# Kernel optimization log

Measured on AMD Instinct MI355X. Metric: run time of the kernel, lower is better.

## Reference

```python
import jax, jax.numpy as jnp
import numpy as np

N_NODES = 100000
N_EDGES = 600000
IN_F, HID_F, OUT_F = 128, 128, 64


def setup_inputs() -> dict:
    key = jax.random.key(0)
    ks = jax.random.split(key, 12)
    s = 0.05  # small init scale to keep activations bounded
    return {
        "features": jax.random.normal(ks[0], (N_NODES, IN_F), jnp.float32),
        "edge_src": jax.random.randint(ks[1], (N_EDGES,), 0, N_NODES, jnp.int32),
        "edge_dst": jax.random.randint(ks[2], (N_EDGES,), 0, N_NODES, jnp.int32),
        "W1": jax.random.normal(ks[3], (HID_F, 3 * IN_F), jnp.float32) * s,
        "b1": jnp.zeros((HID_F,), jnp.float32),
        "bn_gamma": jnp.ones((HID_F,), jnp.float32),
        "bn_beta": jnp.zeros((HID_F,), jnp.float32),
        "bn_mean": jnp.zeros((HID_F,), jnp.float32),
        "bn_var": jnp.ones((HID_F,), jnp.float32),
        "W3": jax.random.normal(ks[4], (HID_F, 3 * HID_F), jnp.float32) * s,
        "b3": jnp.zeros((HID_F,), jnp.float32),
        "Wm1": jax.random.normal(ks[5], (HID_F, HID_F), jnp.float32) * s,
        "bm1": jnp.zeros((HID_F,), jnp.float32),
        "Wm2": jax.random.normal(ks[6], (OUT_F, HID_F), jnp.float32) * s,
        "bm2": jnp.zeros((OUT_F,), jnp.float32),
    }


def _cheb_conv(x, W, b, src, dst, dinv, n):
    """DGL ChebConv with k=3, lambda_max=2 (re_norm=1).
    L f = f - D^-1/2 A D^-1/2 f  via gather-scatter on the edge list."""
    def lap(f):
        agg = jax.ops.segment_sum((f * dinv)[src], dst, num_segments=n)
        return f - agg * dinv
    X0 = x
    X1 = -lap(X0)                 # X1 = -re_norm*L(X0) + (re_norm-1)*X0, re_norm=1
    X2 = -2.0 * lap(X1) - X0      # X2 = -2*re_norm*L(X1) + 2*(re_norm-1)*X1 - X0
    Xt = jnp.concatenate([X0, X1, X2], axis=1)  # [n, 3*in]
    return Xt @ W.T + b


def reference(features, edge_src, edge_dst, W1, b1, bn_gamma, bn_beta,
              bn_mean, bn_var, W3, b3, Wm1, bm1, Wm2, bm2):
    n = features.shape[0]
    deg = jax.ops.segment_sum(jnp.ones_like(edge_dst, jnp.float32), edge_dst,
                              num_segments=n)
    dinv = jnp.clip(deg, 1.0, None) ** -0.5  # D^{-1/2}, in-degree (DGL)
    dinv = dinv[:, None]

    x = jax.nn.relu(_cheb_conv(features, W1, b1, edge_src, edge_dst, dinv, n))
    # BatchNorm1d (eval mode)
    x = (x - bn_mean) * jax.lax.rsqrt(bn_var + 1e-5) * bn_gamma + bn_beta
    # NOTE: original early-stopping loop never updates x -> dead code, omitted.
    x_res = x
    x = jax.nn.relu(_cheb_conv(x, W3, b3, edge_src, edge_dst, dinv, n))
    x = x + x_res  # dropout is identity in eval mode
    # MLP head
    h = jax.nn.relu(x @ Wm1.T + bm1)
    return h @ Wm2.T + bm2
```

## Files before the change

### kernel.cpp

```cpp
#include <hip/hip_runtime.h>
#include <cstdint>
#include <cstddef>

#define NF 128
#define SCAN_B 256

typedef __attribute__((ext_vector_type(4))) float f32x4;
typedef __attribute__((ext_vector_type(8))) short bf16x8;

#define GL2LDS16(g, l) __builtin_amdgcn_global_load_lds(                     \
    (const __attribute__((address_space(1))) unsigned*)(g),                  \
    (__attribute__((address_space(3))) unsigned*)(l), 16, 0, 0)

static __device__ inline float bf2f(short u) {
    union { unsigned u; float f; } v;
    v.u = ((unsigned)(unsigned short)u) << 16;
    return v.f;
}
static __device__ inline short f2bf(float f) {
    union { float f; unsigned u; } v; v.f = f;
    unsigned r = v.u + 0x7FFF + ((v.u >> 16) & 1);
    return (short)(r >> 16);
}
static __device__ inline float u2f(unsigned u) {
    union { unsigned u; float f; } v; v.u = u; return v.f;
}
static __device__ inline unsigned f2u(float f) {
    union { float f; unsigned u; } v; v.f = f; return v.u;
}
static __device__ inline unsigned packbf(float lo, float hi) {
    unsigned ul = f2u(lo), uh = f2u(hi);
    ul = ul + 0x7FFF + ((ul >> 16) & 1);
    uh = uh + 0x7FFF + ((uh >> 16) & 1);
    return (ul >> 16) | (uh & 0xFFFF0000u);
}


static __global__ __launch_bounds__(256) void k_pro(
    const int* __restrict__ dst, int ne, int* __restrict__ counts,
    const float* __restrict__ feat, short* __restrict__ fbf, int n8, int nbE, int nbF,
    const float* __restrict__ w1, const float* __restrict__ w3,
    const float* __restrict__ wm1, const float* __restrict__ wm2,
    short* __restrict__ o1, short* __restrict__ o3,
    short* __restrict__ om1, short* __restrict__ om2) {
    int b = blockIdx.x;
    if (b < nbE) {
        int e = b * 256 + threadIdx.x;
        if (e < ne) atomicAdd(&counts[dst[e]], 1);
        return;
    }
    b -= nbE;
    if (b < nbF) {
        int i = b * 256 + threadIdx.x;
        if (i < n8) {
            f32x4 a = *(const f32x4*)&feat[(size_t)i * 8];
            f32x4 c = *(const f32x4*)&feat[(size_t)i * 8 + 4];
            bf16x8 r;
            r[0] = f2bf(a[0]); r[1] = f2bf(a[1]); r[2] = f2bf(a[2]); r[3] = f2bf(a[3]);
            r[4] = f2bf(c[0]); r[5] = f2bf(c[1]); r[6] = f2bf(c[2]); r[7] = f2bf(c[3]);
            *(bf16x8*)&fbf[(size_t)i * 8] = r;
        }
        return;
    }
    b -= nbF;
    int i = b * 256 + threadIdx.x;
    if (i < 12288) {
        const float* x = (i < 6144) ? w1 : w3;
        short* y       = (i < 6144) ? o1 : o3;
        int ii = (i < 6144) ? i : i - 6144;
        int r = ii / 48, c = ii % 48;
        int kt = c * 8, seg = kt >> 7, o = kt & 127;
        const float* base = x + (size_t)r * 384;
        float c0, c1, c2;
        if (seg == 0)      { c0 = 1.f;  c1 = -1.f; c2 = 1.f;  }
        else if (seg == 1) { c0 = 0.f;  c1 = 1.f;  c2 = -4.f; }
        else               { c0 = 0.f;  c1 = 0.f;  c2 = 2.f;  }
        bf16x8 rr;
#pragma unroll
        for (int h = 0; h < 2; ++h) {
            f32x4 a0 = *(const f32x4*)&base[o + h * 4];
            f32x4 a1 = *(const f32x4*)&base[128 + o + h * 4];
            f32x4 a2 = *(const f32x4*)&base[256 + o + h * 4];
#pragma unroll
            for (int j = 0; j < 4; ++j)
                rr[h * 4 + j] = f2bf(c0 * a0[j] + c1 * a1[j] + c2 * a2[j]);
        }
        *(bf16x8*)&y[(size_t)r * 384 + kt] = rr;
        return;
    }
    const float* x; short* y; int off;
    if (i < 14336) { x = wm1; y = om1; off = i - 12288; }
    else           { x = wm2; y = om2; off = i - 14336; }
    f32x4 a = *(const f32x4*)&x[(size_t)off * 8];
    f32x4 c = *(const f32x4*)&x[(size_t)off * 8 + 4];
    bf16x8 r;
    r[0] = f2bf(a[0]); r[1] = f2bf(a[1]); r[2] = f2bf(a[2]); r[3] = f2bf(a[3]);
    r[4] = f2bf(c[0]); r[5] = f2bf(c[1]); r[6] = f2bf(c[2]); r[7] = f2bf(c[3]);
    *(bf16x8*)&y[(size_t)off * 8] = r;
}


static __global__ void k_scan1(const int* __restrict__ counts, int n,
                               int* __restrict__ row_off, int* __restrict__ bsum) {
    __shared__ int s[SCAN_B];
    int t = threadIdx.x;
    int base = blockIdx.x * SCAN_B;
    int v = (base + t < n) ? counts[base + t] : 0;
    s[t] = v;
    __syncthreads();
    for (int off = 1; off < SCAN_B; off <<= 1) {
        int x = 0;
        if (t >= off) x = s[t - off];
        __syncthreads();
        if (t >= off) s[t] += x;
        __syncthreads();
    }
    if (base + t < n) row_off[base + t] = s[t] - v;
    if (t == SCAN_B - 1) bsum[blockIdx.x] = s[t];
}

static __global__ void k_scan2(int* __restrict__ bsum, int nb) {
    __shared__ int s[512];
    int t = threadIdx.x;
    int v = (t < nb) ? bsum[t] : 0;
    s[t] = v;
    __syncthreads();
    for (int off = 1; off < 512; off <<= 1) {
        int x = 0;
        if (t >= off) x = s[t - off];
        __syncthreads();
        if (t >= off) s[t] += x;
        __syncthreads();
    }
    if (t < nb) bsum[t] = s[t] - v;
}

static __global__ void k_scan3(int* __restrict__ row_off, const int* __restrict__ bsum,
                               int n, int ne, int* __restrict__ cursor,
                               const int* __restrict__ counts, float* __restrict__ dinv) {
    int i = blockIdx.x * SCAN_B + threadIdx.x;
    if (i < n) {
        int v = row_off[i] + bsum[blockIdx.x];
        row_off[i] = v;
        cursor[i] = v;
        float d = fmaxf((float)counts[i], 1.0f);
        dinv[i] = rsqrtf(d);
    }
    if (i == 0) row_off[n] = ne;
}

static __global__ void k_fill(const int* __restrict__ src, const int* __restrict__ dst, int ne,
                              int* __restrict__ cursor, int* __restrict__ csr) {
    int e = blockIdx.x * blockDim.x + threadIdx.x;
    if (e < ne) {
        int d = dst[e];
        int p = atomicAdd(&cursor[d], 1);
        csr[p] = src[e];
    }
}


static __global__ __launch_bounds__(256) void k_lap(
    const short* __restrict__ Xin,
    const int* __restrict__ row_off, const int* __restrict__ csr,
    const float* __restrict__ dinv,
    short* __restrict__ out, int n) {
    int node = blockIdx.x * 4 + (threadIdx.x >> 6);
    if (node >= n) return;
    int l = threadIdx.x & 63;
    const unsigned* Xu = (const unsigned*)Xin;
    int e0 = row_off[node], e1 = row_off[node + 1];
    int deg = e1 - e0;

    int myi = 0;
    float mydv = 0.f;
    if (l < deg && l < 64) {
        myi = csr[e0 + l];
        mydv = dinv[myi];
    }

    float s0 = 0.f, s1 = 0.f;
    int dcap = deg < 64 ? deg : 64;
    for (int base = 0; base < dcap; base += 8) {
        unsigned v[8]; float dv[8];
#pragma unroll
        for (int j = 0; j < 8; ++j) {
            int jj = base + j;
            bool act = (jj < dcap);
            int lane = act ? jj : base;
            int src = __builtin_amdgcn_readlane(myi, lane);
            unsigned dvb = __builtin_amdgcn_readlane((int)f2u(mydv), lane);
            dv[j] = act ? u2f(dvb) : 0.f;
            v[j] = Xu[(size_t)src * 64 + l];
        }
#pragma unroll
        for (int j = 0; j < 8; ++j) {
            s0 += u2f(v[j] << 16) * dv[j];
            s1 += u2f(v[j] & 0xFFFF0000u) * dv[j];
        }
    }
    for (int base = e0 + 64; base < e1; base += 8) {
        int m = e1 - base;
        int idx = 0;
        if (l < 8 && l < m) idx = csr[base + l];
        unsigned v[8]; float dv[8];
#pragma unroll
        for (int j = 0; j < 8; ++j) {
            int src = __shfl(idx, j, 64);
            bool act = (j < m);
            if (!act) src = 0;
            dv[j] = act ? dinv[src] : 0.f;
            v[j] = Xu[(size_t)src * 64 + l];
        }
#pragma unroll
        for (int j = 0; j < 8; ++j) {
            s0 += u2f(v[j] << 16) * dv[j];
            s1 += u2f(v[j] & 0xFFFF0000u) * dv[j];
        }
    }

    float di = dinv[node];
    ((unsigned*)out)[(size_t)node * 64 + l] = packbf(s0 * di, s1 * di);
}


static __global__ __launch_bounds__(512) void k_gemm_conv(
    const short* __restrict__ X0, const short* __restrict__ X1, const short* __restrict__ X2,
    const short* __restrict__ Wbf, const float* __restrict__ bias,
    const short* __restrict__ res,
    const float* __restrict__ bng, const float* __restrict__ bnb,
    const float* __restrict__ bnm, const float* __restrict__ bnv,
    int M, int mode, short* __restrict__ out) {
    __shared__ short As[2][128 * 32];
    __shared__ short Bs[2][128 * 32];

    const int nwg = gridDim.x;
    const int q = nwg >> 3, r = nwg & 7;
    const int xcd = blockIdx.x & 7, slot = blockIdx.x >> 3;
    const int flat = (xcd < r ? xcd * (q + 1) : r * (q + 1) + (xcd - r) * q) + slot;
    const int m0 = flat * 128;

    const int t = threadIdx.x;
    const int wv = t >> 6;
    const int ln = t & 63;
    const int wr = wv >> 2;
    const int wc = wv & 3;
    const int lr = ln & 15;
    const int lk = ln >> 4;

    const short* segs[3] = {X0, X1, X2};

    f32x4 acc[4][2];
#pragma unroll
    for (int i = 0; i < 4; ++i)
#pragma unroll
        for (int j = 0; j < 2; ++j) acc[i][j] = (f32x4){0.f, 0.f, 0.f, 0.f};

    auto issue = [&](int buf, int kt) {
        const short* Xp = segs[kt >> 7];
        const int klocal = kt & 127;
#pragma unroll
        for (int j = 0; j < 2; ++j) {
            int g = wv * 2 + j;
            int c = g * 64 + ln;
            if (g < 8) {
                int row = c >> 2, sl = c & 3;
                int gm = m0 + row;
                if (gm > M - 1) gm = M - 1;
                const short* src = &Xp[(size_t)gm * 128 + klocal + ((sl ^ ((row >> 1) & 3)) * 8)];
                GL2LDS16(src, &As[buf][g * 512]);
            } else {
                int cb = c - 512;
                int row = cb >> 2, sl = cb & 3;
                const short* src = &Wbf[(size_t)row * 384 + kt + ((sl ^ ((row >> 1) & 3)) * 8)];
                GL2LDS16(src, &Bs[buf][(g - 8) * 512]);
            }
        }
    };
    auto compute = [&](int buf) {
        bf16x8 af[4], bfr[2];
#pragma unroll
        for (int fi = 0; fi < 4; ++fi) {
            int row = wr * 64 + fi * 16 + lr;
            af[fi] = *(const bf16x8*)&As[buf][row * 32 + ((lk ^ ((row >> 1) & 3)) * 8)];
        }
#pragma unroll
        for (int fj = 0; fj < 2; ++fj) {
            int row = wc * 32 + fj * 16 + lr;
            bfr[fj] = *(const bf16x8*)&Bs[buf][row * 32 + ((lk ^ ((row >> 1) & 3)) * 8)];
        }
#pragma unroll
        for (int fi = 0; fi < 4; ++fi)
#pragma unroll
            for (int fj = 0; fj < 2; ++fj)
                acc[fi][fj] = __builtin_amdgcn_mfma_f32_16x16x32_bf16(af[fi], bfr[fj], acc[fi][fj], 0, 0, 0);
    };

    issue(0, 0);
    __syncthreads();
#pragma unroll
    for (int tgt = 0; tgt < 12; ++tgt) {
        if (tgt < 11) issue((tgt + 1) & 1, (tgt + 1) * 32);
        compute(tgt & 1);
        __syncthreads();
    }

#pragma unroll
    for (int fi = 0; fi < 4; ++fi) {
#pragma unroll
        for (int reg = 0; reg < 4; ++reg) {
            int gm = m0 + wr * 64 + fi * 16 + lk * 4 + reg;
            if (gm >= M) continue;
#pragma unroll
            for (int fj = 0; fj < 2; ++fj) {
                int gn = wc * 32 + fj * 16 + lr;
                float y = acc[fi][fj][reg] + bias[gn];
                y = fmaxf(y, 0.f);
                if (mode == 2) {
                    float sc = rsqrtf(bnv[gn] + 1e-5f) * bng[gn];
                    y = (y - bnm[gn]) * sc + bnb[gn];
                } else {
                    y += bf2f(res[(size_t)gm * 128 + gn]);
                }
                out[(size_t)gm * 128 + gn] = f2bf(y);
            }
        }
    }
}


#define LDP 40

static __global__ __launch_bounds__(256) void k_mlp(
    const short* __restrict__ X, const short* __restrict__ Wm1bf, const float* __restrict__ bm1,
    const short* __restrict__ Wm2bf, const float* __restrict__ bm2,
    int M, float* __restrict__ out) {
    __shared__ short As[64 * LDP];
    __shared__ short Bs[128 * LDP];
    __shared__ short hs[64 * 136];

    const int t = threadIdx.x;
    const int m0 = blockIdx.x * 64;
    const int w  = t >> 6;
    const int wr = w >> 1;
    const int wc = w & 1;
    const int l  = t & 63;
    const int lr = l & 15;
    const int lk = l >> 4;

    f32x4 acc1[2][4];
#pragma unroll
    for (int i = 0; i < 2; ++i)
#pragma unroll
        for (int j = 0; j < 4; ++j) acc1[i][j] = (f32x4){0.f, 0.f, 0.f, 0.f};

    for (int kt = 0; kt < 128; kt += 32) {
        {
            int row = t >> 2;
            int slot = t & 3;
            int gm = m0 + row;
            bf16x8 v = {0, 0, 0, 0, 0, 0, 0, 0};
            if (gm < M) v = *(const bf16x8*)&X[(size_t)gm * 128 + kt + slot * 8];
            *(bf16x8*)&As[row * LDP + slot * 8] = v;
        }
#pragma unroll
        for (int it = 0; it < 2; ++it) {
            int idx = it * 256 + t;
            int row = idx >> 2;
            int slot = idx & 3;
            bf16x8 v = *(const bf16x8*)&Wm1bf[(size_t)row * 128 + kt + slot * 8];
            *(bf16x8*)&Bs[row * LDP + slot * 8] = v;
        }
        __syncthreads();

        bf16x8 af[2], bfr[4];
#pragma unroll
        for (int fi = 0; fi < 2; ++fi)
            af[fi] = *(const bf16x8*)&As[(wr * 32 + fi * 16 + lr) * LDP + lk * 8];
#pragma unroll
        for (int fj = 0; fj < 4; ++fj)
            bfr[fj] = *(const bf16x8*)&Bs[(wc * 64 + fj * 16 + lr) * LDP + lk * 8];
#pragma unroll
        for (int fi = 0; fi < 2; ++fi)
#pragma unroll
            for (int fj = 0; fj < 4; ++fj)
                acc1[fi][fj] = __builtin_amdgcn_mfma_f32_16x16x32_bf16(af[fi], bfr[fj], acc1[fi][fj], 0, 0, 0);
        __syncthreads();
    }

#pragma unroll
    for (int fi = 0; fi < 2; ++fi) {
#pragma unroll
        for (int reg = 0; reg < 4; ++reg) {
            int rloc = wr * 32 + fi * 16 + lk * 4 + reg;
#pragma unroll
            for (int fj = 0; fj < 4; ++fj) {
                int col = wc * 64 + fj * 16 + lr;
                float y = acc1[fi][fj][reg] + bm1[col];
                hs[rloc * 136 + col] = f2bf(fmaxf(y, 0.f));
            }
        }
    }
    __syncthreads();

    f32x4 acc2[2][2];
#pragma unroll
    for (int i = 0; i < 2; ++i)
#pragma unroll
        for (int j = 0; j < 2; ++j) acc2[i][j] = (f32x4){0.f, 0.f, 0.f, 0.f};

    for (int kt = 0; kt < 128; kt += 32) {
        {
            int row = t >> 2;
            int slot = t & 3;
            bf16x8 v = *(const bf16x8*)&Wm2bf[(size_t)row * 128 + kt + slot * 8];
            *(bf16x8*)&As[row * LDP + slot * 8] = v;
        }
        __syncthreads();

        bf16x8 af[2], bfr[2];
#pragma unroll
        for (int fi = 0; fi < 2; ++fi)
            af[fi] = *(const bf16x8*)&hs[(wr * 32 + fi * 16 + lr) * 136 + kt + lk * 8];
#pragma unroll
        for (int fj = 0; fj < 2; ++fj)
            bfr[fj] = *(const bf16x8*)&As[(wc * 32 + fj * 16 + lr) * LDP + lk * 8];
#pragma unroll
        for (int fi = 0; fi < 2; ++fi)
#pragma unroll
            for (int fj = 0; fj < 2; ++fj)
                acc2[fi][fj] = __builtin_amdgcn_mfma_f32_16x16x32_bf16(af[fi], bfr[fj], acc2[fi][fj], 0, 0, 0);
        __syncthreads();
    }

#pragma unroll
    for (int fi = 0; fi < 2; ++fi) {
#pragma unroll
        for (int reg = 0; reg < 4; ++reg) {
            int gm = m0 + wr * 32 + fi * 16 + lk * 4 + reg;
            if (gm >= M) continue;
#pragma unroll
            for (int fj = 0; fj < 2; ++fj) {
                int gn = wc * 32 + fj * 16 + lr;
                out[(size_t)gm * 64 + gn] = acc2[fi][fj][reg] + bm2[gn];
            }
        }
    }
}


extern "C" void kernel_launch(void* const* d_in, const int* in_sizes, int n_in,
                              void* d_out, int out_size, void* d_ws, size_t ws_size,
                              hipStream_t stream) {
    const float* features = (const float*)d_in[0];
    const int*   esrc     = (const int*)d_in[1];
    const int*   edst     = (const int*)d_in[2];
    const float* W1   = (const float*)d_in[3];
    const float* b1   = (const float*)d_in[4];
    const float* bng  = (const float*)d_in[5];
    const float* bnb  = (const float*)d_in[6];
    const float* bnm  = (const float*)d_in[7];
    const float* bnv  = (const float*)d_in[8];
    const float* W3   = (const float*)d_in[9];
    const float* b3   = (const float*)d_in[10];
    const float* Wm1  = (const float*)d_in[11];
    const float* bm1  = (const float*)d_in[12];
    const float* Wm2  = (const float*)d_in[13];
    const float* bm2  = (const float*)d_in[14];
    float* out = (float*)d_out;

    const int n  = in_sizes[0] / NF;
    const int ne = in_sizes[1];

    uint8_t* w = (uint8_t*)d_ws;
    size_t off = 0;
    auto alloc = [&](size_t bytes) -> void* {
        void* p = w + off;
        off = (off + bytes + 255) & ~(size_t)255;
        return p;
    };
    float* dinv   = (float*)alloc((size_t)n * 4);
    int* counts   = (int*)alloc((size_t)n * 4);
    int* row_off  = (int*)alloc(((size_t)n + 1) * 4);
    int* cursor   = (int*)alloc((size_t)n * 4);
    int* csr      = (int*)alloc((size_t)ne * 4);
    int* bsum     = (int*)alloc(4096);
    short* fbf    = (short*)alloc((size_t)n * NF * 2);
    short* bufB   = (short*)alloc((size_t)n * NF * 2);
    short* bufC   = (short*)alloc((size_t)n * NF * 2);
    short* bufD   = (short*)alloc((size_t)n * NF * 2);
    short* bufE   = (short*)alloc((size_t)n * NF * 2);
    short* W1bf   = (short*)alloc((size_t)128 * 384 * 2);
    short* W3bf   = (short*)alloc((size_t)128 * 384 * 2);
    short* Wm1bf  = (short*)alloc((size_t)128 * 128 * 2);
    short* Wm2bf  = (short*)alloc((size_t)64 * 128 * 2);
    (void)ws_size;

    const int TB = 256;
    const int nbE = (ne + TB - 1) / TB;
    const int nbN = (n + TB - 1) / TB;
    const int n8  = n * NF / 8;
    const int nbF = (n8 + TB - 1) / TB;

    hipMemsetAsync(counts, 0, (size_t)n * 4, stream);
    k_pro<<<nbE + nbF + 60, TB, 0, stream>>>(edst, ne, counts,
                                             features, fbf, n8, nbE, nbF,
                                             W1, W3, Wm1, Wm2, W1bf, W3bf, Wm1bf, Wm2bf);
    k_scan1<<<nbN, SCAN_B, 0, stream>>>(counts, n, row_off, bsum);
    k_scan2<<<1, 512, 0, stream>>>(bsum, nbN);
    k_scan3<<<nbN, SCAN_B, 0, stream>>>(row_off, bsum, n, ne, cursor, counts, dinv);
    k_fill<<<nbE, TB, 0, stream>>>(esrc, edst, ne, cursor, csr);

    const int gm128 = (n + 127) / 128;
    const int gm64  = (n + 63) / 64;
    const int nbL   = (n + 3) / 4;

    k_lap<<<nbL, 256, 0, stream>>>(fbf, row_off, csr, dinv, bufB, n);
    k_lap<<<nbL, 256, 0, stream>>>(bufB, row_off, csr, dinv, bufC, n);
    k_gemm_conv<<<gm128, 512, 0, stream>>>(fbf, bufB, bufC, W1bf, b1,
                                           nullptr, bng, bnb, bnm, bnv, n, 2, bufD);

    k_lap<<<nbL, 256, 0, stream>>>(bufD, row_off, csr, dinv, bufB, n);
    k_lap<<<nbL, 256, 0, stream>>>(bufB, row_off, csr, dinv, bufC, n);
    k_gemm_conv<<<gm128, 512, 0, stream>>>(bufD, bufB, bufC, W3bf, b3,
                                           bufD, nullptr, nullptr, nullptr, nullptr, n, 3, bufE);

    k_mlp<<<gm64, 256, 0, stream>>>(bufE, Wm1bf, bm1, Wm2bf, bm2, n, out);
}
```

Measured before the change: 317.5 us.

## Fuse second Cheb GEMM with MLP head and pack dinv into CSR

Merges the second ChebConv GEMM (bias, relu, residual) with both MLP layers in one kernel. The hidden activations stay in LDS instead of being written to and re-read from a global buffer, and one launch is removed. Separately, the CSR entries now store the source index together with that source's dinv value, so the Laplacian gather no longer does a dependent dinv lookup per edge. The cost is a larger CSR array (8 bytes per edge), more LDS and register pressure in the fused kernel, and the gemm_conv kernel is specialised to the batch-norm mode only.

```diff
diff --git a/kernel.cpp b/kernel.cpp
--- a/kernel.cpp
+++ b/kernel.cpp
@@ -150,19 +150,21 @@
 }
 
 static __global__ void k_fill(const int* __restrict__ src, const int* __restrict__ dst, int ne,
-                              int* __restrict__ cursor, int* __restrict__ csr) {
+                              int* __restrict__ cursor, int2* __restrict__ csrw,
+                              const float* __restrict__ dinv) {
     int e = blockIdx.x * blockDim.x + threadIdx.x;
     if (e < ne) {
         int d = dst[e];
+        int s = src[e];
         int p = atomicAdd(&cursor[d], 1);
-        csr[p] = src[e];
+        csrw[p] = make_int2(s, (int)f2u(dinv[s]));
     }
 }
 
 
 static __global__ __launch_bounds__(256) void k_lap(
     const short* __restrict__ Xin,
-    const int* __restrict__ row_off, const int* __restrict__ csr,
+    const int* __restrict__ row_off, const int2* __restrict__ csrw,
     const float* __restrict__ dinv,
     short* __restrict__ out, int n) {
     int node = blockIdx.x * 4 + (threadIdx.x >> 6);
@@ -172,11 +174,10 @@
     int e0 = row_off[node], e1 = row_off[node + 1];
     int deg = e1 - e0;
 
-    int myi = 0;
-    float mydv = 0.f;
+    int myi = 0; int mydv = 0;
     if (l < deg && l < 64) {
-        myi = csr[e0 + l];
-        mydv = dinv[myi];
+        int2 q = csrw[e0 + l];
+        myi = q.x; mydv = q.y;
     }
 
     float s0 = 0.f, s1 = 0.f;
@@ -189,7 +190,7 @@
             bool act = (jj < dcap);
             int lane = act ? jj : base;
             int src = __builtin_amdgcn_readlane(myi, lane);
-            unsigned dvb = __builtin_amdgcn_readlane((int)f2u(mydv), lane);
+            unsigned dvb = __builtin_amdgcn_readlane(mydv, lane);
             dv[j] = act ? u2f(dvb) : 0.f;
             v[j] = Xu[(size_t)src * 64 + l];
         }
@@ -201,15 +202,16 @@
     }
     for (int base = e0 + 64; base < e1; base += 8) {
         int m = e1 - base;
-        int idx = 0;
-        if (l < 8 && l < m) idx = csr[base + l];
+        int2 qq = make_int2(0, 0);
+        if (l < 8 && l < m) qq = csrw[base + l];
         unsigned v[8]; float dv[8];
 #pragma unroll
         for (int j = 0; j < 8; ++j) {
-            int src = __shfl(idx, j, 64);
+            int src = __shfl(qq.x, j, 64);
+            int dvb = __shfl(qq.y, j, 64);
             bool act = (j < m);
             if (!act) src = 0;
-            dv[j] = act ? dinv[src] : 0.f;
+            dv[j] = act ? u2f((unsigned)dvb) : 0.f;
             v[j] = Xu[(size_t)src * 64 + l];
         }
 #pragma unroll
@@ -227,10 +229,9 @@
 static __global__ __launch_bounds__(512) void k_gemm_conv(
     const short* __restrict__ X0, const short* __restrict__ X1, const short* __restrict__ X2,
     const short* __restrict__ Wbf, const float* __restrict__ bias,
-    const short* __restrict__ res,
     const float* __restrict__ bng, const float* __restrict__ bnb,
     const float* __restrict__ bnm, const float* __restrict__ bnv,
-    int M, int mode, short* __restrict__ out) {
+    int M, short* __restrict__ out) {
     __shared__ short As[2][128 * 32];
     __shared__ short Bs[2][128 * 32];
 
@@ -314,14 +315,9 @@
 #pragma unroll
             for (int fj = 0; fj < 2; ++fj) {
                 int gn = wc * 32 + fj * 16 + lr;
-                float y = acc[fi][fj][reg] + bias[gn];
-                y = fmaxf(y, 0.f);
-                if (mode == 2) {
-                    float sc = rsqrtf(bnv[gn] + 1e-5f) * bng[gn];
-                    y = (y - bnm[gn]) * sc + bnb[gn];
-                } else {
-                    y += bf2f(res[(size_t)gm * 128 + gn]);
-                }
+                float y = fmaxf(acc[fi][fj][reg] + bias[gn], 0.f);
+                float sc = rsqrtf(bnv[gn] + 1e-5f) * bng[gn];
+                y = (y - bnm[gn]) * sc + bnb[gn];
                 out[(size_t)gm * 128 + gn] = f2bf(y);
             }
         }
@@ -329,121 +325,198 @@
 }
 
 
-#define LDP 40
-
-static __global__ __launch_bounds__(256) void k_mlp(
-    const short* __restrict__ X, const short* __restrict__ Wm1bf, const float* __restrict__ bm1,
+static __global__ __launch_bounds__(512) void k_gemm_mlp(
+    const short* __restrict__ X0, const short* __restrict__ X1, const short* __restrict__ X2,
+    const short* __restrict__ Wbf, const float* __restrict__ bias,
+    const short* __restrict__ res,
+    const short* __restrict__ Wm1bf, const float* __restrict__ bm1,
     const short* __restrict__ Wm2bf, const float* __restrict__ bm2,
     int M, float* __restrict__ out) {
-    __shared__ short As[64 * LDP];
-    __shared__ short Bs[128 * LDP];
-    __shared__ short hs[64 * 136];
+    __shared__ __align__(16) short smem[25600];
+    short* As0 = smem;
+    short* As1 = smem + 4096;
+    short* Bs0 = smem + 8192;
+    short* Bs1 = smem + 12288;
+    short* hs  = smem;
+    short* Wst = smem + 17408;
+
+    const int nwg = gridDim.x;
+    const int q = nwg >> 3, r = nwg & 7;
+    const int xcd = blockIdx.x & 7, slot = blockIdx.x >> 3;
+    const int flat = (xcd < r ? xcd * (q + 1) : r * (q + 1) + (xcd - r) * q) + slot;
+    const int m0 = flat * 128;
 
     const int t = threadIdx.x;
-    const int m0 = blockIdx.x * 64;
-    const int w  = t >> 6;
-    const int wr = w >> 1;
-    const int wc = w & 1;
-    const int l  = t & 63;
-    const int lr = l & 15;
-    const int lk = l >> 4;
-
-    f32x4 acc1[2][4];
-#pragma unroll
-    for (int i = 0; i < 2; ++i)
-#pragma unroll
-        for (int j = 0; j < 4; ++j) acc1[i][j] = (f32x4){0.f, 0.f, 0.f, 0.f};
-
-    for (int kt = 0; kt < 128; kt += 32) {
-        {
-            int row = t >> 2;
-            int slot = t & 3;
+    const int wv = t >> 6;
+    const int ln = t & 63;
+    const int wr = wv >> 2;
+    const int wc = wv & 3;
+    const int lr = ln & 15;
+    const int lk = ln >> 4;
+
+    const short* segs[3] = {X0, X1, X2};
+
+    f32x4 acc[4][2];
+#pragma unroll
+    for (int i = 0; i < 4; ++i)
+#pragma unroll
+        for (int j = 0; j < 2; ++j) acc[i][j] = (f32x4){0.f, 0.f, 0.f, 0.f};
+
+    auto issue = [&](int buf, int kt) {
+        const short* Xp = segs[kt >> 7];
+        const int klocal = kt & 127;
+        short* Ab = buf ? As1 : As0;
+        short* Bb = buf ? Bs1 : Bs0;
+#pragma unroll
+        for (int j = 0; j < 2; ++j) {
+            int g = wv * 2 + j;
+            int c = g * 64 + ln;
+            if (g < 8) {
+                int row = c >> 2, sl = c & 3;
+                int gm = m0 + row;
+                if (gm > M - 1) gm = M - 1;
+                const short* src = &Xp[(size_t)gm * 128 + klocal + ((sl ^ ((row >> 1) & 3)) * 8)];
+                GL2LDS16(src, &Ab[g * 512]);
+            } else {
+                int cb = c - 512;
+                int row = cb >> 2, sl = cb & 3;
+                const short* src = &Wbf[(size_t)row * 384 + kt + ((sl ^ ((row >> 1) & 3)) * 8)];
+                GL2LDS16(src, &Bb[(g - 8) * 512]);
+            }
+        }
+    };
+    auto compute = [&](int buf) {
+        short* Ab = buf ? As1 : As0;
+        short* Bb = buf ? Bs1 : Bs0;
+        bf16x8 af[4], bfr[2];
+#pragma unroll
+        for (int fi = 0; fi < 4; ++fi) {
+            int row = wr * 64 + fi * 16 + lr;
+            af[fi] = *(const bf16x8*)&Ab[row * 32 + ((lk ^ ((row >> 1) & 3)) * 8)];
+        }
+#pragma unroll
+        for (int fj = 0; fj < 2; ++fj) {
+            int row = wc * 32 + fj * 16 + lr;
+            bfr[fj] = *(const bf16x8*)&Bb[row * 32 + ((lk ^ ((row >> 1) & 3)) * 8)];
+        }
+#pragma unroll
+        for (int fi = 0; fi < 4; ++fi)
+#pragma unroll
+            for (int fj = 0; fj < 2; ++fj)
+                acc[fi][fj] = __builtin_amdgcn_mfma_f32_16x16x32_bf16(af[fi], bfr[fj], acc[fi][fj], 0, 0, 0);
+    };
+
+    issue(0, 0);
+    __syncthreads();
+#pragma unroll
+    for (int tgt = 0; tgt < 12; ++tgt) {
+        if (tgt < 11) issue((tgt + 1) & 1, (tgt + 1) * 32);
+        compute(tgt & 1);
+        __syncthreads();
+    }
+
+    auto issueW1 = [&](int buf, int kt) {
+        int c = t;
+        int row = c >> 2, sl = c & 3;
+        const short* src = &Wm1bf[(size_t)row * 128 + kt + ((sl ^ ((row >> 1) & 3)) * 8)];
+        GL2LDS16(src, &Wst[buf * 4096 + c * 8]);
+    };
+    issueW1(0, 0);
+
+#pragma unroll
+    for (int fi = 0; fi < 4; ++fi) {
+#pragma unroll
+        for (int reg = 0; reg < 4; ++reg) {
+            int row = wr * 64 + fi * 16 + lk * 4 + reg;
             int gm = m0 + row;
-            bf16x8 v = {0, 0, 0, 0, 0, 0, 0, 0};
-            if (gm < M) v = *(const bf16x8*)&X[(size_t)gm * 128 + kt + slot * 8];
-            *(bf16x8*)&As[row * LDP + slot * 8] = v;
-        }
-#pragma unroll
-        for (int it = 0; it < 2; ++it) {
-            int idx = it * 256 + t;
-            int row = idx >> 2;
-            int slot = idx & 3;
-            bf16x8 v = *(const bf16x8*)&Wm1bf[(size_t)row * 128 + kt + slot * 8];
-            *(bf16x8*)&Bs[row * LDP + slot * 8] = v;
-        }
-        __syncthreads();
-
-        bf16x8 af[2], bfr[4];
-#pragma unroll
-        for (int fi = 0; fi < 2; ++fi)
-            af[fi] = *(const bf16x8*)&As[(wr * 32 + fi * 16 + lr) * LDP + lk * 8];
-#pragma unroll
-        for (int fj = 0; fj < 4; ++fj)
-            bfr[fj] = *(const bf16x8*)&Bs[(wc * 64 + fj * 16 + lr) * LDP + lk * 8];
-#pragma unroll
-        for (int fi = 0; fi < 2; ++fi)
-#pragma unroll
-            for (int fj = 0; fj < 4; ++fj)
-                acc1[fi][fj] = __builtin_amdgcn_mfma_f32_16x16x32_bf16(af[fi], bfr[fj], acc1[fi][fj], 0, 0, 0);
-        __syncthreads();
-    }
-
-#pragma unroll
-    for (int fi = 0; fi < 2; ++fi) {
-#pragma unroll
-        for (int reg = 0; reg < 4; ++reg) {
-            int rloc = wr * 32 + fi * 16 + lk * 4 + reg;
-#pragma unroll
-            for (int fj = 0; fj < 4; ++fj) {
-                int col = wc * 64 + fj * 16 + lr;
-                float y = acc1[fi][fj][reg] + bm1[col];
-                hs[rloc * 136 + col] = f2bf(fmaxf(y, 0.f));
-            }
-        }
-    }
-    __syncthreads();
-
-    f32x4 acc2[2][2];
-#pragma unroll
-    for (int i = 0; i < 2; ++i)
-#pragma unroll
-        for (int j = 0; j < 2; ++j) acc2[i][j] = (f32x4){0.f, 0.f, 0.f, 0.f};
-
-    for (int kt = 0; kt < 128; kt += 32) {
-        {
-            int row = t >> 2;
-            int slot = t & 3;
-            bf16x8 v = *(const bf16x8*)&Wm2bf[(size_t)row * 128 + kt + slot * 8];
-            *(bf16x8*)&As[row * LDP + slot * 8] = v;
-        }
-        __syncthreads();
-
-        bf16x8 af[2], bfr[2];
-#pragma unroll
-        for (int fi = 0; fi < 2; ++fi)
-            af[fi] = *(const bf16x8*)&hs[(wr * 32 + fi * 16 + lr) * 136 + kt + lk * 8];
-#pragma unroll
-        for (int fj = 0; fj < 2; ++fj)
-            bfr[fj] = *(const bf16x8*)&As[(wc * 32 + fj * 16 + lr) * LDP + lk * 8];
-#pragma unroll
-        for (int fi = 0; fi < 2; ++fi)
-#pragma unroll
-            for (int fj = 0; fj < 2; ++fj)
-                acc2[fi][fj] = __builtin_amdgcn_mfma_f32_16x16x32_bf16(af[fi], bfr[fj], acc2[fi][fj], 0, 0, 0);
-        __syncthreads();
-    }
-
-#pragma unroll
-    for (int fi = 0; fi < 2; ++fi) {
-#pragma unroll
-        for (int reg = 0; reg < 4; ++reg) {
-            int gm = m0 + wr * 32 + fi * 16 + lk * 4 + reg;
-            if (gm >= M) continue;
+            int gr = gm < M ? gm : M - 1;
 #pragma unroll
             for (int fj = 0; fj < 2; ++fj) {
                 int gn = wc * 32 + fj * 16 + lr;
-                out[(size_t)gm * 64 + gn] = acc2[fi][fj][reg] + bm2[gn];
+                float y = fmaxf(acc[fi][fj][reg] + bias[gn], 0.f) + bf2f(res[(size_t)gr * 128 + gn]);
+                hs[row * 136 + gn] = f2bf(y);
             }
+        }
+    }
+    __syncthreads();
+
+    f32x4 acc2[4][2];
+#pragma unroll
+    for (int i = 0; i < 4; ++i)
+#pragma unroll
+        for (int j = 0; j < 2; ++j) acc2[i][j] = (f32x4){0.f, 0.f, 0.f, 0.f};
+
+#pragma unroll
+    for (int s = 0; s < 4; ++s) {
+        if (s < 3) issueW1((s + 1) & 1, (s + 1) * 32);
+        int kt = s * 32;
+        short* Wb = &Wst[(s & 1) * 4096];
+        bf16x8 af[4], bw[2];
+#pragma unroll
+        for (int fi = 0; fi < 4; ++fi) {
+            int row = wr * 64 + fi * 16 + lr;
+            af[fi] = *(const bf16x8*)&hs[row * 136 + kt + lk * 8];
+        }
+#pragma unroll
+        for (int fj = 0; fj < 2; ++fj) {
+            int row = wc * 32 + fj * 16 + lr;
+            bw[fj] = *(const bf16x8*)&Wb[row * 32 + ((lk ^ ((row >> 1) & 3)) * 8)];
+        }
+#pragma unroll
+        for (int fi = 0; fi < 4; ++fi)
+#pragma unroll
+            for (int fj = 0; fj < 2; ++fj)
+                acc2[fi][fj] = __builtin_amdgcn_mfma_f32_16x16x32_bf16(af[fi], bw[fj], acc2[fi][fj], 0, 0, 0);
+        __syncthreads();
+    }
+
+#pragma unroll
+    for (int j = 0; j < 2; ++j) {
+        int c = j * 512 + t;
+        int row = c >> 4, s = c & 15;
+        const short* src = &Wm2bf[(size_t)row * 128 + ((s ^ (row & 7)) * 8)];
+        GL2LDS16(src, &Wst[c * 8]);
+    }
+#pragma unroll
+    for (int fi = 0; fi < 4; ++fi) {
+#pragma unroll
+        for (int reg = 0; reg < 4; ++reg) {
+            int row = wr * 64 + fi * 16 + lk * 4 + reg;
+#pragma unroll
+            for (int fj = 0; fj < 2; ++fj) {
+                int col = wc * 32 + fj * 16 + lr;
+                hs[row * 136 + col] = f2bf(fmaxf(acc2[fi][fj][reg] + bm1[col], 0.f));
+            }
+        }
+    }
+    __syncthreads();
+
+    f32x4 acc3[4];
+#pragma unroll
+    for (int i = 0; i < 4; ++i) acc3[i] = (f32x4){0.f, 0.f, 0.f, 0.f};
+#pragma unroll
+    for (int s = 0; s < 4; ++s) {
+        int kt = s * 32;
+        bf16x8 af, bw;
+        int brow = wc * 16 + lr;
+        int sidx = s * 4 + lk;
+        bw = *(const bf16x8*)&Wst[brow * 128 + ((sidx ^ (brow & 7)) * 8)];
+#pragma unroll
+        for (int fi = 0; fi < 4; ++fi) {
+            int row = wr * 64 + fi * 16 + lr;
+            af = *(const bf16x8*)&hs[row * 136 + kt + lk * 8];
+            acc3[fi] = __builtin_amdgcn_mfma_f32_16x16x32_bf16(af, bw, acc3[fi], 0, 0, 0);
+        }
+    }
+
+#pragma unroll
+    for (int fi = 0; fi < 4; ++fi) {
+#pragma unroll
+        for (int reg = 0; reg < 4; ++reg) {
+            int gm = m0 + wr * 64 + fi * 16 + lk * 4 + reg;
+            if (gm >= M) continue;
+            int col = wc * 16 + lr;
+            out[(size_t)gm * 64 + col] = acc3[fi][reg] + bm2[col];
         }
     }
 }
@@ -483,13 +556,12 @@
     int* counts   = (int*)alloc((size_t)n * 4);
     int* row_off  = (int*)alloc(((size_t)n + 1) * 4);
     int* cursor   = (int*)alloc((size_t)n * 4);
-    int* csr      = (int*)alloc((size_t)ne * 4);
+    int2* csrw    = (int2*)alloc((size_t)ne * 8);
     int* bsum     = (int*)alloc(4096);
     short* fbf    = (short*)alloc((size_t)n * NF * 2);
     short* bufB   = (short*)alloc((size_t)n * NF * 2);
     short* bufC   = (short*)alloc((size_t)n * NF * 2);
     short* bufD   = (short*)alloc((size_t)n * NF * 2);
-    short* bufE   = (short*)alloc((size_t)n * NF * 2);
     short* W1bf   = (short*)alloc((size_t)128 * 384 * 2);
     short* W3bf   = (short*)alloc((size_t)128 * 384 * 2);
     short* Wm1bf  = (short*)alloc((size_t)128 * 128 * 2);
@@ -509,21 +581,18 @@
     k_scan1<<<nbN, SCAN_B, 0, stream>>>(counts, n, row_off, bsum);
     k_scan2<<<1, 512, 0, stream>>>(bsum, nbN);
     k_scan3<<<nbN, SCAN_B, 0, stream>>>(row_off, bsum, n, ne, cursor, counts, dinv);
-    k_fill<<<nbE, TB, 0, stream>>>(esrc, edst, ne, cursor, csr);
+    k_fill<<<nbE, TB, 0, stream>>>(esrc, edst, ne, cursor, csrw, dinv);
 
     const int gm128 = (n + 127) / 128;
-    const int gm64  = (n + 63) / 64;
     const int nbL   = (n + 3) / 4;
 
-    k_lap<<<nbL, 256, 0, stream>>>(fbf, row_off, csr, dinv, bufB, n);
-    k_lap<<<nbL, 256, 0, stream>>>(bufB, row_off, csr, dinv, bufC, n);
+    k_lap<<<nbL, 256, 0, stream>>>(fbf, row_off, csrw, dinv, bufB, n);
+    k_lap<<<nbL, 256, 0, stream>>>(bufB, row_off, csrw, dinv, bufC, n);
     k_gemm_conv<<<gm128, 512, 0, stream>>>(fbf, bufB, bufC, W1bf, b1,
-                                           nullptr, bng, bnb, bnm, bnv, n, 2, bufD);
-
-    k_lap<<<nbL, 256, 0, stream>>>(bufD, row_off, csr, dinv, bufB, n);
-    k_lap<<<nbL, 256, 0, stream>>>(bufB, row_off, csr, dinv, bufC, n);
-    k_gemm_conv<<<gm128, 512, 0, stream>>>(bufD, bufB, bufC, W3bf, b3,
-                                           bufD, nullptr, nullptr, nullptr, nullptr, n, 3, bufE);
-
-    k_mlp<<<gm64, 256, 0, stream>>>(bufE, Wm1bf, bm1, Wm2bf, bm2, n, out);
-}
+                                           bng, bnb, bnm, bnv, n, bufD);
+
+    k_lap<<<nbL, 256, 0, stream>>>(bufD, row_off, csrw, dinv, bufB, n);
+    k_lap<<<nbL, 256, 0, stream>>>(bufB, row_off, csrw, dinv, bufC, n);
+    k_gemm_mlp<<<gm128, 512, 0, stream>>>(bufD, bufB, bufC, W3bf, b3, bufD,
+                                          Wm1bf, bm1, Wm2bf, bm2, n, out);
+}
```

Measured after the change: 283.2 us. 10.8% less time.
